# Performance work log

Measured on AMD Instinct MI355X. Metric: run time of the kernel, lower is better.

Reference implementation:

```python
import jax, jax.numpy as jnp
import numpy as np

N = 100000
E = 1600000
IN_FEATS = 512
N_CLASSES = 40
H1, D1 = 8, 8
H2, D2 = 1, N_CLASSES


def gat_conv(x, src, dst, W, al, ar, b, H, D):
    # x: [N, F] -> h: [N, H, D]
    n = x.shape[0]
    h = (x @ W).reshape(n, H, D)
    el = (h * al[None]).sum(-1)  # [N, H]
    er = (h * ar[None]).sum(-1)  # [N, H]
    e = jax.nn.leaky_relu(el[src] + er[dst], 0.2)  # [E, H]
    # segment softmax over destination neighborhoods
    emax = jax.ops.segment_max(e, dst, num_segments=n)  # [N, H]
    ee = jnp.exp(e - emax[dst])
    denom = jax.ops.segment_sum(ee, dst, num_segments=n)  # [N, H]
    a = ee / (denom[dst] + 1e-9)  # [E, H]
    m = h[src] * a[:, :, None]  # [E, H, D]
    out = jax.ops.segment_sum(m, dst, num_segments=n)  # [N, H, D]
    return out + b.reshape(1, H, D)


def setup_inputs() -> dict:
    key = jax.random.key(0)
    ks = jax.random.split(key, 12)
    g1 = 1.0 / np.sqrt(IN_FEATS)
    g2 = 1.0 / np.sqrt(H1 * D1)
    return {
        "x": jax.random.normal(ks[0], (N, IN_FEATS), jnp.float32),
        "src": jax.random.randint(ks[1], (E,), 0, N, jnp.int32),
        "dst": jax.random.randint(ks[2], (E,), 0, N, jnp.int32),
        "W1": jax.random.normal(ks[3], (IN_FEATS, H1 * D1), jnp.float32) * g1,
        "al1": jax.random.normal(ks[4], (H1, D1), jnp.float32) * 0.1,
        "ar1": jax.random.normal(ks[5], (H1, D1), jnp.float32) * 0.1,
        "b1": jnp.zeros((H1 * D1,), jnp.float32),
        "W2": jax.random.normal(ks[6], (H1 * D1, H2 * D2), jnp.float32) * g2,
        "al2": jax.random.normal(ks[7], (H2, D2), jnp.float32) * 0.1,
        "ar2": jax.random.normal(ks[8], (H2, D2), jnp.float32) * 0.1,
        "b2": jnp.zeros((H2 * D2,), jnp.float32),
    }


def reference(x, src, dst, W1, al1, ar1, b1, W2, al2, ar2, b2):
    h = gat_conv(x, src, dst, W1, al1, ar1, b1, H1, D1)  # [N, 8, 8]
    h = jax.nn.elu(h.reshape(N, H1 * D1))  # [N, 64]
    h = gat_conv(h, src, dst, W2, al2, ar2, b2, H2, D2).mean(axis=1)  # [N, n_classes]
    return jax.nn.log_softmax(h, axis=1)
```

## Files before the change

### kernel.cpp

```cpp
#include <hip/hip_runtime.h>
#include <hip/hip_bf16.h>
#include <math.h>

#define NCLS 40
#define H2S 64
#define PWG 256
#define BSH 9
#define NBMAX 512
#define SRCB 23
#define CSRCAP 14336

typedef __attribute__((ext_vector_type(8))) short bf16x8;
typedef __attribute__((ext_vector_type(4))) float f32x4;

__device__ inline float bf2f(ushort u) {
    unsigned v = ((unsigned)u) << 16;
    float f;
    __builtin_memcpy(&f, &v, 4);
    return f;
}
__device__ inline ushort f2bf(float f) {
    unsigned v;
    __builtin_memcpy(&v, &f, 4);
    unsigned r = (v + 0x7FFFu + ((v >> 16) & 1u)) >> 16;
    return (ushort)r;
}
__device__ inline unsigned pkbf(float a, float b) {
    unsigned ua, ub;
    __builtin_memcpy(&ua, &a, 4);
    __builtin_memcpy(&ub, &b, 4);
    return __builtin_amdgcn_perm(ub + 0x8000u, ua + 0x8000u, 0x07060302u);
}

__global__ __launch_bounds__(256) void hist_prep_kernel(
    const int* __restrict__ dst, int* __restrict__ hist, int Ee, int chunk, int NB,
    const float* __restrict__ W1, ushort* __restrict__ W1t,
    const float* __restrict__ W2, const float* __restrict__ al2,
    const float* __restrict__ ar2, float* __restrict__ wal2,
    float* __restrict__ war2)
{
    if (blockIdx.x >= PWG) {
        int bb = blockIdx.x - PWG;
        if (bb < 128) {
            int id = bb * 256 + threadIdx.x;
            int k = id >> 6, c = id & 63;
            W1t[c * 512 + k] = f2bf(W1[k * 64 + c]);
        } else if (threadIdx.x < 64) {
            int k = threadIdx.x;
            float a = 0.f, b = 0.f;
            for (int c = 0; c < NCLS; c++) {
                float w = W2[k * NCLS + c];
                a += w * al2[c];
                b += w * ar2[c];
            }
            wal2[k] = a;
            war2[k] = b;
        }
        return;
    }
    __shared__ int lh[NBMAX];
    const int wg = blockIdx.x, tid = threadIdx.x;
    for (int i = tid; i < NB; i += 256) lh[i] = 0;
    __syncthreads();
    const int beg = wg * chunk;
    const int endv = min(Ee, beg + chunk);
    for (int i = beg + tid; i < endv; i += 256) atomicAdd(&lh[dst[i] >> BSH], 1);
    __syncthreads();
    for (int b = tid; b < NB; b += 256) hist[b * PWG + wg] = lh[b];
}

__global__ __launch_bounds__(256) void gemm1_mfma_kernel(
    const float* __restrict__ x, const ushort* __restrict__ W1t,
    const float* __restrict__ al1, const float* __restrict__ ar1,
    ushort* __restrict__ h1b, float* __restrict__ el1,
    float* __restrict__ er1, int Nn)
{
    __shared__ ushort As[64 * 72];
    __shared__ ushort Bs[64 * 72];
    const int t = threadIdx.x;
    const int lane = t & 63, w = t >> 6;
    const int tile = blockIdx.x * 64;

    f32x4 acc[4] = {};

    const int sr = t >> 2;
    const int sk = (t & 3) * 16;
    const int arow = tile + sr;
    const bool rowok = arow < Nn;
    const float* xrow = x + (size_t)arow * 512;
    const ushort* wrow = W1t + (size_t)sr * 512;

    const int r = lane & 15, g = lane >> 4;

    float4 f0 = make_float4(0.f, 0.f, 0.f, 0.f), f1 = f0, f2 = f0, f3 = f0;
    bf16x8 bv0, bv1;
    if (rowok) {
        f0 = *(const float4*)(xrow + sk);
        f1 = *(const float4*)(xrow + sk + 4);
        f2 = *(const float4*)(xrow + sk + 8);
        f3 = *(const float4*)(xrow + sk + 12);
    }
    bv0 = *(const bf16x8*)(wrow + sk);
    bv1 = *(const bf16x8*)(wrow + sk + 8);

    for (int k0 = 0; k0 < 512; k0 += 64) {
        uint4 aw0, aw1;
        aw0.x = pkbf(f0.x, f0.y); aw0.y = pkbf(f0.z, f0.w);
        aw0.z = pkbf(f1.x, f1.y); aw0.w = pkbf(f1.z, f1.w);
        aw1.x = pkbf(f2.x, f2.y); aw1.y = pkbf(f2.z, f2.w);
        aw1.z = pkbf(f3.x, f3.y); aw1.w = pkbf(f3.z, f3.w);
        *(uint4*)&As[sr * 72 + sk] = aw0;
        *(uint4*)&As[sr * 72 + sk + 8] = aw1;
        *(bf16x8*)&Bs[sr * 72 + sk] = bv0;
        *(bf16x8*)&Bs[sr * 72 + sk + 8] = bv1;
        __syncthreads();

        int k1 = k0 + 64;
        if (k1 < 512) {
            if (rowok) {
                f0 = *(const float4*)(xrow + k1 + sk);
                f1 = *(const float4*)(xrow + k1 + sk + 4);
                f2 = *(const float4*)(xrow + k1 + sk + 8);
                f3 = *(const float4*)(xrow + k1 + sk + 12);
            }
            bv0 = *(const bf16x8*)(wrow + k1 + sk);
            bv1 = *(const bf16x8*)(wrow + k1 + sk + 8);
        }

        bf16x8 af0 = *(const bf16x8*)&As[(w * 16 + r) * 72 + g * 8];
        bf16x8 af1 = *(const bf16x8*)&As[(w * 16 + r) * 72 + 32 + g * 8];
#pragma unroll
        for (int cb = 0; cb < 4; cb++) {
            bf16x8 bf0 = *(const bf16x8*)&Bs[(cb * 16 + r) * 72 + g * 8];
            acc[cb] = __builtin_amdgcn_mfma_f32_16x16x32_bf16(af0, bf0, acc[cb], 0, 0, 0);
        }
#pragma unroll
        for (int cb = 0; cb < 4; cb++) {
            bf16x8 bf1 = *(const bf16x8*)&Bs[(cb * 16 + r) * 72 + 32 + g * 8];
            acc[cb] = __builtin_amdgcn_mfma_f32_16x16x32_bf16(af1, bf1, acc[cb], 0, 0, 0);
        }
        __syncthreads();
    }

    float alv[4], arv[4];
#pragma unroll
    for (int cb = 0; cb < 4; cb++) {
        alv[cb] = al1[cb * 16 + r];
        arv[cb] = ar1[cb * 16 + r];
    }
#pragma unroll
    for (int v = 0; v < 4; v++) {
        int row = tile + w * 16 + g * 4 + v;
        bool ok = row < Nn;
#pragma unroll
        for (int cb = 0; cb < 4; cb++) {
            if (ok) h1b[(size_t)row * 64 + cb * 16 + r] = f2bf(acc[cb][v]);
            float pel = acc[cb][v] * alv[cb];
            float per = acc[cb][v] * arv[cb];
            pel += __shfl_xor(pel, 1); per += __shfl_xor(per, 1);
            pel += __shfl_xor(pel, 2); per += __shfl_xor(per, 2);
            pel += __shfl_xor(pel, 4); per += __shfl_xor(per, 4);
            if (ok && (r & 7) == 0) {
                int head = cb * 2 + (r >> 3);
                el1[row * 8 + head] = pel;
                er1[row * 8 + head] = per;
            }
        }
    }
}

__global__ __launch_bounds__(256) void scanA_kernel(int* __restrict__ hist,
                                                    int* __restrict__ bucketTot)
{
    __shared__ int s[256];
    const int b = blockIdx.x, tid = threadIdx.x;
    int v = hist[b * PWG + tid];
    s[tid] = v;
    __syncthreads();
#pragma unroll
    for (int o = 1; o < 256; o <<= 1) {
        int t = (tid >= o) ? s[tid - o] : 0;
        __syncthreads();
        s[tid] += t;
        __syncthreads();
    }
    hist[b * PWG + tid] = s[tid] - v;
    if (tid == 255) bucketTot[b] = s[255];
}

__global__ __launch_bounds__(256) void scanB_kernel(const int* __restrict__ bucketTot,
                                                    int* __restrict__ bucketBase,
                                                    int NB, int Ee)
{
    __shared__ int s[256];
    const int tid = threadIdx.x;
    int v = (tid < NB) ? bucketTot[tid] : 0;
    s[tid] = v;
    __syncthreads();
#pragma unroll
    for (int o = 1; o < 256; o <<= 1) {
        int t = (tid >= o) ? s[tid - o] : 0;
        __syncthreads();
        s[tid] += t;
        __syncthreads();
    }
    if (tid < NB) bucketBase[tid] = s[tid] - v;
    if (tid == 0) bucketBase[NB] = Ee;
}

__global__ __launch_bounds__(256) void partition_kernel(const int* __restrict__ src,
                                                        const int* __restrict__ dst,
                                                        const int* __restrict__ hist,
                                                        const int* __restrict__ bucketBase,
                                                        unsigned* __restrict__ ebuf,
                                                        int Ee, int chunk, int NB)
{
    __shared__ int cur[NBMAX];
    const int wg = blockIdx.x, tid = threadIdx.x;
    for (int b = tid; b < NB; b += 256) cur[b] = hist[b * PWG + wg] + bucketBase[b];
    __syncthreads();
    const int beg = wg * chunk;
    const int endv = min(Ee, beg + chunk);
    for (int i = beg + tid; i < endv; i += 256) {
        int d = dst[i];
        int p = atomicAdd(&cur[d >> BSH], 1);
        ebuf[p] = ((unsigned)(d & ((1 << BSH) - 1)) << SRCB) | (unsigned)src[i];
    }
}

__global__ __launch_bounds__(512) void bucket_csr_kernel(const unsigned* __restrict__ ebuf,
                                                         const int* __restrict__ bucketBase,
                                                         int* __restrict__ row_start,
                                                         int* __restrict__ perm_src,
                                                         int Nn, int Ee, int NB)
{
    __shared__ unsigned stage[CSRCAP];
    __shared__ int cnt[512];
    __shared__ int s[512];
    __shared__ int cur[512];
    const int b = blockIdx.x, tid = threadIdx.x;
    const int base = b << BSH;
    const int bb = bucketBase[b], be = bucketBase[b + 1];
    const int m = be - bb;

    cnt[tid] = 0;
    __syncthreads();
    for (int idx = tid; idx < m; idx += 512) {
        unsigned pk = ebuf[bb + idx];
        if (idx < CSRCAP) stage[idx] = pk;
        atomicAdd(&cnt[pk >> SRCB], 1);
    }
    __syncthreads();
    int v = cnt[tid];
    s[tid] = v;
    __syncthreads();
#pragma unroll
    for (int o = 1; o < 512; o <<= 1) {
        int t = (tid >= o) ? s[tid - o] : 0;
        __syncthreads();
        s[tid] += t;
        __syncthreads();
    }
    const int off = bb + s[tid] - v;
    const int node = base + tid;
    if (node < Nn) row_start[node] = off;
    cur[tid] = off;
    __syncthreads();
    for (int idx = tid; idx < m; idx += 512) {
        unsigned pk = (idx < CSRCAP) ? stage[idx] : ebuf[bb + idx];
        int p = atomicAdd(&cur[pk >> SRCB], 1);
        perm_src[p] = (int)(pk & ((1u << SRCB) - 1u));
    }
    if (b == NB - 1 && tid == 0) row_start[Nn] = Ee;
}

__global__ __launch_bounds__(256) void agg1_kernel(
    const ushort* __restrict__ h1b, const float* __restrict__ el1,
    const float* __restrict__ er1, const int* __restrict__ row_start,
    const int* __restrict__ perm_src, const float* __restrict__ b1,
    ushort* __restrict__ hmidb, int Nn)
{
    const int wid = (blockIdx.x * blockDim.x + threadIdx.x) >> 6;
    const int lane = threadIdx.x & 63;
    if (wid >= Nn) return;
    const int g = lane >> 4;
    const int q = lane & 15;
    const int h = q >> 1;
    const int beg = row_start[wid], end = row_start[wid + 1];
    const float er = er1[wid * 8 + h];

    float a0 = 0.f, a1 = 0.f, a2 = 0.f, a3 = 0.f, denom = 0.f;
    for (int i0 = beg; i0 < end; i0 += 64) {
        const int cnt = min(end - i0, 64);
        int pv = (i0 + lane < end) ? perm_src[i0 + lane] : 0;
        for (int j = 0; j < cnt; j += 8) {
            const int e0 = j + g, e1 = j + 4 + g;
            const int s0 = __shfl(pv, min(e0, cnt - 1));
            const int s1 = __shfl(pv, min(e1, cnt - 1));
            ushort4 r0 = *(const ushort4*)&h1b[(size_t)s0 * 64 + q * 4];
            ushort4 r1 = *(const ushort4*)&h1b[(size_t)s1 * 64 + q * 4];
            float x0 = el1[s0 * 8 + h];
            float x1 = el1[s1 * 8 + h];
            float e = x0 + er;
            e = (e >= 0.f) ? e : 0.2f * e;
            float w0 = (e0 < cnt) ? __expf(e) : 0.f;
            e = x1 + er;
            e = (e >= 0.f) ? e : 0.2f * e;
            float w1 = (e1 < cnt) ? __expf(e) : 0.f;
            denom += w0 + w1;
            a0 += bf2f(r0.x) * w0 + bf2f(r1.x) * w1;
            a1 += bf2f(r0.y) * w0 + bf2f(r1.y) * w1;
            a2 += bf2f(r0.z) * w0 + bf2f(r1.z) * w1;
            a3 += bf2f(r0.w) * w0 + bf2f(r1.w) * w1;
        }
    }
    denom += __shfl_xor(denom, 16); denom += __shfl_xor(denom, 32);
    a0 += __shfl_xor(a0, 16); a0 += __shfl_xor(a0, 32);
    a1 += __shfl_xor(a1, 16); a1 += __shfl_xor(a1, 32);
    a2 += __shfl_xor(a2, 16); a2 += __shfl_xor(a2, 32);
    a3 += __shfl_xor(a3, 16); a3 += __shfl_xor(a3, 32);
    if (g == 0) {
        const float4 bv = *(const float4*)&b1[q * 4];
        const float inv = 1.f / (denom + 1e-9f);
        float v0 = a0 * inv + bv.x;
        float v1 = a1 * inv + bv.y;
        float v2 = a2 * inv + bv.z;
        float v3 = a3 * inv + bv.w;
        v0 = (v0 > 0.f) ? v0 : expm1f(v0);
        v1 = (v1 > 0.f) ? v1 : expm1f(v1);
        v2 = (v2 > 0.f) ? v2 : expm1f(v2);
        v3 = (v3 > 0.f) ? v3 : expm1f(v3);
        uint2 o;
        o.x = pkbf(v0, v1);
        o.y = pkbf(v2, v3);
        *(uint2*)&hmidb[(size_t)wid * 64 + q * 4] = o;
    }
}

__global__ __launch_bounds__(256) void gemm2_kernel(
    const ushort* __restrict__ hmidb, const float* __restrict__ W2,
    const float* __restrict__ wal2, const float* __restrict__ war2,
    ushort* __restrict__ h2b, int Nn)
{
    __shared__ float w2s[64 * NCLS];
    __shared__ float wals[64], wars[64];
    for (int i = threadIdx.x; i < 64 * NCLS; i += blockDim.x) w2s[i] = W2[i];
    if (threadIdx.x < 64) {
        wals[threadIdx.x] = wal2[threadIdx.x];
        wars[threadIdx.x] = war2[threadIdx.x];
    }
    __syncthreads();
    int n = blockIdx.x * blockDim.x + threadIdx.x;
    if (n >= Nn) return;

    float out[NCLS];
#pragma unroll
    for (int c = 0; c < NCLS; c++) out[c] = 0.f;
    float accel = 0.f, accer = 0.f;

#pragma unroll 4
    for (int k4 = 0; k4 < 16; k4++) {
        ushort4 u = *(const ushort4*)&hmidb[(size_t)n * 64 + k4 * 4];
        float h0 = bf2f(u.x), h1 = bf2f(u.y), h2 = bf2f(u.z), h3 = bf2f(u.w);
        accel += h0 * wals[k4 * 4] + h1 * wals[k4 * 4 + 1] + h2 * wals[k4 * 4 + 2] + h3 * wals[k4 * 4 + 3];
        accer += h0 * wars[k4 * 4] + h1 * wars[k4 * 4 + 1] + h2 * wars[k4 * 4 + 2] + h3 * wars[k4 * 4 + 3];
#pragma unroll
        for (int c = 0; c < NCLS; c++) {
            out[c] += h0 * w2s[(k4 * 4 + 0) * NCLS + c] + h1 * w2s[(k4 * 4 + 1) * NCLS + c] +
                      h2 * w2s[(k4 * 4 + 2) * NCLS + c] + h3 * w2s[(k4 * 4 + 3) * NCLS + c];
        }
    }
    ushort* row = h2b + (size_t)n * H2S;
#pragma unroll
    for (int c = 0; c < NCLS; c += 2) {
        *(unsigned*)&row[c] = pkbf(out[c], out[c + 1]);
    }
    ((float*)row)[20] = accel;
    ((float*)row)[21] = accer;
}

__global__ __launch_bounds__(256) void agg2_kernel(
    const ushort* __restrict__ h2b, const int* __restrict__ row_start,
    const int* __restrict__ perm_src, const float* __restrict__ b2,
    float* __restrict__ out, int Nn)
{
    const int wid = (blockIdx.x * blockDim.x + threadIdx.x) >> 6;
    const int lane = threadIdx.x & 63;
    if (wid >= Nn) return;
    const int g = lane >> 4;
    const int q = lane & 15;
    const int beg = row_start[wid], end = row_start[wid + 1];
    const float er = ((const float*)(h2b + (size_t)wid * H2S))[21];

    float a0 = 0.f, a1 = 0.f, a2 = 0.f, a3 = 0.f, denom = 0.f;
    for (int i0 = beg; i0 < end; i0 += 64) {
        const int cnt = min(end - i0, 64);
        int pv = (i0 + lane < end) ? perm_src[i0 + lane] : 0;
        for (int j = 0; j < cnt; j += 8) {
            const int e0 = j + g, e1 = j + 4 + g;
            const int s0 = __shfl(pv, min(e0, cnt - 1));
            const int s1 = __shfl(pv, min(e1, cnt - 1));
            const ushort* rp0 = h2b + (size_t)s0 * H2S;
            const ushort* rp1 = h2b + (size_t)s1 * H2S;
            ushort4 r0 = *(const ushort4*)(rp0 + q * 4);
            ushort4 r1 = *(const ushort4*)(rp1 + q * 4);
            float x0 = ((const float*)rp0)[20];
            float x1 = ((const float*)rp1)[20];
            float e = x0 + er;
            e = (e >= 0.f) ? e : 0.2f * e;
            float w0 = (e0 < cnt) ? __expf(e) : 0.f;
            e = x1 + er;
            e = (e >= 0.f) ? e : 0.2f * e;
            float w1 = (e1 < cnt) ? __expf(e) : 0.f;
            denom += w0 + w1;
            a0 += bf2f(r0.x) * w0 + bf2f(r1.x) * w1;
            a1 += bf2f(r0.y) * w0 + bf2f(r1.y) * w1;
            a2 += bf2f(r0.z) * w0 + bf2f(r1.z) * w1;
            a3 += bf2f(r0.w) * w0 + bf2f(r1.w) * w1;
        }
    }
    denom += __shfl_xor(denom, 16); denom += __shfl_xor(denom, 32);
    a0 += __shfl_xor(a0, 16); a0 += __shfl_xor(a0, 32);
    a1 += __shfl_xor(a1, 16); a1 += __shfl_xor(a1, 32);
    a2 += __shfl_xor(a2, 16); a2 += __shfl_xor(a2, 32);
    a3 += __shfl_xor(a3, 16); a3 += __shfl_xor(a3, 32);

    const bool act = (g == 0) && (q < 10);
    float v0, v1, v2, v3;
    if (act) {
        const float4 bv = *(const float4*)&b2[q * 4];
        const float inv = 1.f / (denom + 1e-9f);
        v0 = a0 * inv + bv.x;
        v1 = a1 * inv + bv.y;
        v2 = a2 * inv + bv.z;
        v3 = a3 * inv + bv.w;
    } else {
        v0 = v1 = v2 = v3 = -1e30f;
    }
    float mx = fmaxf(fmaxf(v0, v1), fmaxf(v2, v3));
#pragma unroll
    for (int o = 1; o < 64; o <<= 1) mx = fmaxf(mx, __shfl_xor(mx, o));
    float sx = act ? (__expf(v0 - mx) + __expf(v1 - mx) + __expf(v2 - mx) + __expf(v3 - mx)) : 0.f;
#pragma unroll
    for (int o = 1; o < 64; o <<= 1) sx += __shfl_xor(sx, o);
    if (act) {
        float lg = mx + __logf(sx);
        float4 o4 = make_float4(v0 - lg, v1 - lg, v2 - lg, v3 - lg);
        *(float4*)&out[(size_t)wid * NCLS + q * 4] = o4;
    }
}

extern "C" void kernel_launch(void* const* d_in, const int* in_sizes, int n_in,
                              void* d_out, int out_size, void* d_ws, size_t ws_size,
                              hipStream_t stream)
{
    const float* x   = (const float*)d_in[0];
    const int*   src = (const int*)d_in[1];
    const int*   dst = (const int*)d_in[2];
    const float* W1  = (const float*)d_in[3];
    const float* al1 = (const float*)d_in[4];
    const float* ar1 = (const float*)d_in[5];
    const float* b1  = (const float*)d_in[6];
    const float* W2  = (const float*)d_in[7];
    const float* al2 = (const float*)d_in[8];
    const float* ar2 = (const float*)d_in[9];
    const float* b2  = (const float*)d_in[10];
    float* out = (float*)d_out;

    const int Nn = in_sizes[0] / 512;
    const int Ee = in_sizes[1];
    const int NB = (Nn + (1 << BSH) - 1) >> BSH;
    const int chunk = (Ee + PWG - 1) / PWG;

    char* wsb = (char*)d_ws;
    size_t off = 0;
    auto alloc = [&](size_t bytes) -> void* {
        off = (off + 15) & ~(size_t)15;
        void* p = wsb + off;
        off += bytes;
        return p;
    };
    ushort* h1b   = (ushort*)alloc((size_t)Nn * 64 * 2);
    ushort* hmidb = (ushort*)alloc((size_t)Nn * 64 * 2);
    ushort* h2b   = (ushort*)alloc((size_t)Nn * H2S * 2);
    ushort* W1t   = (ushort*)alloc(64 * 512 * 2);
    float* el1  = (float*)alloc((size_t)Nn * 8 * 4);
    float* er1  = (float*)alloc((size_t)Nn * 8 * 4);
    float* wal2 = (float*)alloc(64 * 4);
    float* war2 = (float*)alloc(64 * 4);
    int* row_start  = (int*)alloc((size_t)(Nn + 1) * 4);
    int* hist       = (int*)alloc((size_t)NB * PWG * 4);
    int* bucketTot  = (int*)alloc((size_t)NB * 4);
    int* bucketBase = (int*)alloc((size_t)(NB + 1) * 4);
    int* perm_src   = (int*)alloc((size_t)Ee * 4);
    unsigned* ebuf  = (unsigned*)alloc((size_t)Ee * 4);

    hist_prep_kernel<<<PWG + 129, 256, 0, stream>>>(dst, hist, Ee, chunk, NB,
                                                    W1, W1t, W2, al2, ar2, wal2, war2);
    scanA_kernel<<<NB, 256, 0, stream>>>(hist, bucketTot);
    scanB_kernel<<<1, 256, 0, stream>>>(bucketTot, bucketBase, NB, Ee);
    partition_kernel<<<PWG, 256, 0, stream>>>(src, dst, hist, bucketBase, ebuf, Ee, chunk, NB);
    bucket_csr_kernel<<<NB, 512, 0, stream>>>(ebuf, bucketBase, row_start, perm_src, Nn, Ee, NB);

    gemm1_mfma_kernel<<<(Nn + 63) / 64, 256, 0, stream>>>(x, W1t, al1, ar1, h1b, el1, er1, Nn);
    agg1_kernel<<<(Nn + 3) / 4, 256, 0, stream>>>(h1b, el1, er1, row_start, perm_src, b1, hmidb, Nn);

    gemm2_kernel<<<(Nn + 255) / 256, 256, 0, stream>>>(hmidb, W2, wal2, war2, h2b, Nn);
    agg2_kernel<<<(Nn + 3) / 4, 256, 0, stream>>>(h2b, row_start, perm_src, b2, out, Nn);
}
```

Before: 240.7 us.

## Fuse partition with GEMM1 launch and inline bucket-base scans

Drops the single-block scanB kernel. Each consumer now recomputes the prefix sum over bucket totals in shared memory, both the partition blocks and every bucket_csr block. The partition work and the GEMM1 tiles are merged into one launch, with the first PWG blocks partitioning edges and the rest computing GEMM1, so the two independent stages overlap and two launch gaps disappear. In exchange, the 256-wide scan is repeated in many blocks, and the merged blocks share one shared-memory footprint.

```diff
diff --git a/kernel.cpp b/kernel.cpp
--- a/kernel.cpp
+++ b/kernel.cpp
@@ -69,7 +69,29 @@
     for (int b = tid; b < NB; b += 256) hist[b * PWG + wg] = lh[b];
 }
 
-__global__ __launch_bounds__(256) void gemm1_mfma_kernel(
+__global__ __launch_bounds__(256) void scanA_kernel(int* __restrict__ hist,
+                                                    int* __restrict__ bucketTot)
+{
+    __shared__ int s[256];
+    const int b = blockIdx.x, tid = threadIdx.x;
+    int v = hist[b * PWG + tid];
+    s[tid] = v;
+    __syncthreads();
+#pragma unroll
+    for (int o = 1; o < 256; o <<= 1) {
+        int t = (tid >= o) ? s[tid - o] : 0;
+        __syncthreads();
+        s[tid] += t;
+        __syncthreads();
+    }
+    hist[b * PWG + tid] = s[tid] - v;
+    if (tid == 255) bucketTot[b] = s[255];
+}
+
+__global__ __launch_bounds__(256) void part_gemm1_kernel(
+    const int* __restrict__ src, const int* __restrict__ dst,
+    const int* __restrict__ hist, const int* __restrict__ bucketTot,
+    unsigned* __restrict__ ebuf, int Ee, int chunk, int NB,
     const float* __restrict__ x, const ushort* __restrict__ W1t,
     const float* __restrict__ al1, const float* __restrict__ ar1,
     ushort* __restrict__ h1b, float* __restrict__ el1,
@@ -77,9 +99,36 @@
 {
     __shared__ ushort As[64 * 72];
     __shared__ ushort Bs[64 * 72];
+
+    if (blockIdx.x < PWG) {
+        int* cur = (int*)As;
+        int* stmp = (int*)Bs;
+        const int wg = blockIdx.x, tid = threadIdx.x;
+        int v = (tid < NB) ? bucketTot[tid] : 0;
+        stmp[tid] = v;
+        __syncthreads();
+#pragma unroll
+        for (int o = 1; o < 256; o <<= 1) {
+            int t = (tid >= o) ? stmp[tid - o] : 0;
+            __syncthreads();
+            stmp[tid] += t;
+            __syncthreads();
+        }
+        if (tid < NB) cur[tid] = hist[tid * PWG + wg] + (stmp[tid] - v);
+        __syncthreads();
+        const int beg = wg * chunk;
+        const int endv = min(Ee, beg + chunk);
+        for (int i = beg + tid; i < endv; i += 256) {
+            int d = dst[i];
+            int p = atomicAdd(&cur[d >> BSH], 1);
+            ebuf[p] = ((unsigned)(d & ((1 << BSH) - 1)) << SRCB) | (unsigned)src[i];
+        }
+        return;
+    }
+
     const int t = threadIdx.x;
     const int lane = t & 63, w = t >> 6;
-    const int tile = blockIdx.x * 64;
+    const int tile = (blockIdx.x - PWG) * 64;
 
     f32x4 acc[4] = {};
 
@@ -169,67 +218,8 @@
     }
 }
 
-__global__ __launch_bounds__(256) void scanA_kernel(int* __restrict__ hist,
-                                                    int* __restrict__ bucketTot)
-{
-    __shared__ int s[256];
-    const int b = blockIdx.x, tid = threadIdx.x;
-    int v = hist[b * PWG + tid];
-    s[tid] = v;
-    __syncthreads();
-#pragma unroll
-    for (int o = 1; o < 256; o <<= 1) {
-        int t = (tid >= o) ? s[tid - o] : 0;
-        __syncthreads();
-        s[tid] += t;
-        __syncthreads();
-    }
-    hist[b * PWG + tid] = s[tid] - v;
-    if (tid == 255) bucketTot[b] = s[255];
-}
-
-__global__ __launch_bounds__(256) void scanB_kernel(const int* __restrict__ bucketTot,
-                                                    int* __restrict__ bucketBase,
-                                                    int NB, int Ee)
-{
-    __shared__ int s[256];
-    const int tid = threadIdx.x;
-    int v = (tid < NB) ? bucketTot[tid] : 0;
-    s[tid] = v;
-    __syncthreads();
-#pragma unroll
-    for (int o = 1; o < 256; o <<= 1) {
-        int t = (tid >= o) ? s[tid - o] : 0;
-        __syncthreads();
-        s[tid] += t;
-        __syncthreads();
-    }
-    if (tid < NB) bucketBase[tid] = s[tid] - v;
-    if (tid == 0) bucketBase[NB] = Ee;
-}
-
-__global__ __launch_bounds__(256) void partition_kernel(const int* __restrict__ src,
-                                                        const int* __restrict__ dst,
-                                                        const int* __restrict__ hist,
-                                                        const int* __restrict__ bucketBase,
-                                                        unsigned* __restrict__ ebuf,
-                                                        int Ee, int chunk, int NB)
-{
-    __shared__ int cur[NBMAX];
-    const int wg = blockIdx.x, tid = threadIdx.x;
-    for (int b = tid; b < NB; b += 256) cur[b] = hist[b * PWG + wg] + bucketBase[b];
-    __syncthreads();
-    const int beg = wg * chunk;
-    const int endv = min(Ee, beg + chunk);
-    for (int i = beg + tid; i < endv; i += 256) {
-        int d = dst[i];
-        int p = atomicAdd(&cur[d >> BSH], 1);
-        ebuf[p] = ((unsigned)(d & ((1 << BSH) - 1)) << SRCB) | (unsigned)src[i];
-    }
-}
-
 __global__ __launch_bounds__(512) void bucket_csr_kernel(const unsigned* __restrict__ ebuf,
-                                                         const int* __restrict__ bucketBase,
+                                                         const int* __restrict__ bucketTot,
                                                          int* __restrict__ row_start,
                                                          int* __restrict__ perm_src,
                                                          int Nn, int Ee, int NB)
@@ -238,9 +228,21 @@
     __shared__ int cnt[512];
     __shared__ int s[512];
     __shared__ int cur[512];
+    __shared__ int bt[256];
     const int b = blockIdx.x, tid = threadIdx.x;
     const int base = b << BSH;
-    const int bb = bucketBase[b], be = bucketBase[b + 1];
+
+    if (tid < 256) bt[tid] = (tid < NB) ? bucketTot[tid] : 0;
+    __syncthreads();
+#pragma unroll
+    for (int o = 1; o < 256; o <<= 1) {
+        int t = (tid >= o && tid < 256) ? bt[tid - o] : 0;
+        __syncthreads();
+        if (tid < 256) bt[tid] += t;
+        __syncthreads();
+    }
+    const int be = bt[b];
+    const int bb = be - bucketTot[b];
     const int m = be - bb;
 
     cnt[tid] = 0;
@@ -491,18 +493,17 @@
     int* row_start  = (int*)alloc((size_t)(Nn + 1) * 4);
     int* hist       = (int*)alloc((size_t)NB * PWG * 4);
     int* bucketTot  = (int*)alloc((size_t)NB * 4);
-    int* bucketBase = (int*)alloc((size_t)(NB + 1) * 4);
     int* perm_src   = (int*)alloc((size_t)Ee * 4);
     unsigned* ebuf  = (unsigned*)alloc((size_t)Ee * 4);
 
     hist_prep_kernel<<<PWG + 129, 256, 0, stream>>>(dst, hist, Ee, chunk, NB,
                                                     W1, W1t, W2, al2, ar2, wal2, war2);
     scanA_kernel<<<NB, 256, 0, stream>>>(hist, bucketTot);
-    scanB_kernel<<<1, 256, 0, stream>>>(bucketTot, bucketBase, NB, Ee);
-    partition_kernel<<<PWG, 256, 0, stream>>>(src, dst, hist, bucketBase, ebuf, Ee, chunk, NB);
-    bucket_csr_kernel<<<NB, 512, 0, stream>>>(ebuf, bucketBase, row_start, perm_src, Nn, Ee, NB);
-
-    gemm1_mfma_kernel<<<(Nn + 63) / 64, 256, 0, stream>>>(x, W1t, al1, ar1, h1b, el1, er1, Nn);
+    part_gemm1_kernel<<<PWG + (Nn + 63) / 64, 256, 0, stream>>>(
+        src, dst, hist, bucketTot, ebuf, Ee, chunk, NB,
+        x, W1t, al1, ar1, h1b, el1, er1, Nn);
+    bucket_csr_kernel<<<NB, 512, 0, stream>>>(ebuf, bucketTot, row_start, perm_src, Nn, Ee, NB);
+
     agg1_kernel<<<(Nn + 3) / 4, 256, 0, stream>>>(h1b, el1, er1, row_start, perm_src, b1, hmidb, Nn);
 
     gemm2_kernel<<<(Nn + 255) / 256, 256, 0, stream>>>(hmidb, W2, wal2, war2, h2b, Nn);
```

Result: faster. 225.9 us (-6.1%).
